# Kernel tuning notes

Measured on AMD Instinct MI355X. Metric: run time of the kernel, lower is better.

The kernel has to match this reference:

```python
import jax, jax.numpy as jnp
import numpy as np

B, D, C = 8192, 128, 1000
EPS = 1e-6      # torch nn.PairwiseDistance default eps (added to the difference)
LAMBD = 0.1


def setup_inputs() -> dict:
    key = jax.random.key(0)
    k1, k2, k3 = jax.random.split(key, 3)
    return {
        "data": jax.random.normal(k1, (B, C), jnp.float32),
        "x": jax.random.normal(k2, (B, D), jnp.float32),
        "y": jax.random.randint(k3, (B,), 0, C),
    }


def _pdist_matrix(x):
    # torch PairwiseDistance(p=2): ||x_i - x_j + eps||_2, computed without
    # materializing the [B,B,D] difference tensor.
    sq = jnp.sum(x * x, axis=1)          # [B]
    s = jnp.sum(x, axis=1)               # [B]
    n = x.shape[1]
    g = x @ x.T                          # [B,B] Gram
    d2 = (sq[:, None] + sq[None, :] - 2.0 * g
          + 2.0 * EPS * (s[:, None] - s[None, :]) + n * EPS * EPS)
    return jnp.sqrt(jnp.maximum(d2, 0.0))


def reference(data, x, y):
    # cross-entropy (mean reduction, as nn.CrossEntropyLoss default)
    logp = jax.nn.log_softmax(data, axis=-1)
    loss_acc = -jnp.mean(jnp.take_along_axis(logp, y[:, None], axis=1))

    dist = _pdist_matrix(x)                       # [B,B]
    same = y[:, None] == y[None, :]               # label mask
    first_pos = jnp.argmax(same, axis=1)          # first index with same label (pos[0] in torch)
    d_pos = jnp.take_along_axis(dist, first_pos[:, None], axis=1)[:, 0]  # [B]
    d_tot = jnp.sum(dist, axis=1)                 # [B]
    loss_feature = jnp.sum(d_pos / (d_tot - d_pos))

    loss = loss_acc + LAMBD * loss_feature
    return (loss, loss_acc, loss_feature)
```

## Files before the change

### kernel.cpp

```cpp
#include <hip/hip_runtime.h>
#include <math.h>

#define B 8192
#define D 128
#define C 1000
#define EPS 1e-6f
#define LAMBD 0.1f

#define OFF_DTOT 2
#define OFF_E (2 + B)
#define OFF_F (2 + 2 * B)
#define OFF_DPOS (2 + 3 * B)
#define OFF_FO (2 + 4 * B)
#define OFF_XBF 33792

typedef __attribute__((ext_vector_type(8))) short short8;
typedef __attribute__((ext_vector_type(4))) float floatx4;

__device__ inline unsigned short f2bf(float f) {
    union { float f; unsigned u; } v; v.f = f;
    unsigned u = v.u;
    return (unsigned short)((u + 0x7fffu + ((u >> 16) & 1u)) >> 16);
}

__global__ void __launch_bounds__(256)
k_rowstats(const float* __restrict__ x, const int* __restrict__ y, float* ws) {
    int row = blockIdx.x * 4 + (threadIdx.x >> 6);
    int lane = threadIdx.x & 63;
    const float2* x2 = (const float2*)x;
    float2 v = x2[row * 64 + lane];
    float sq = v.x * v.x + v.y * v.y;
    float s = v.x + v.y;
    for (int o = 32; o; o >>= 1) {
        sq += __shfl_xor(sq, o);
        s += __shfl_xor(s, o);
    }
    ushort2 p = { f2bf(v.x), f2bf(v.y) };
    ushort2* xrow = (ushort2*)((unsigned short*)(ws + OFF_XBF) + row * 128);
    xrow[(((lane >> 2) ^ (row & 7)) << 2) + (lane & 3)] = p;
    if (lane == 0) {
        ws[OFF_E + row] = sq + 2.f * EPS * s;
        ws[OFF_F + row] = sq - 2.f * EPS * s;
        atomicMin((unsigned*)(ws + OFF_FO) + y[row], (unsigned)row);
    }
}

__global__ void __launch_bounds__(256)
k_ce(const float* __restrict__ data, const int* __restrict__ y, float* ws) {
    int row = blockIdx.x * 4 + (threadIdx.x >> 6);
    int lane = threadIdx.x & 63;
    const float* dr = data + (size_t)row * C;
    const float4* dr4 = (const float4*)dr;

    float4 v[4];
    float m = -1e30f;
#pragma unroll
    for (int k = 0; k < 4; k++) {
        int idx = k * 64 + lane;
        if (idx < C / 4) {
            v[k] = dr4[idx];
            m = fmaxf(fmaxf(fmaxf(m, v[k].x), fmaxf(v[k].y, v[k].z)), v[k].w);
        }
    }
    for (int o = 32; o; o >>= 1) m = fmaxf(m, __shfl_xor(m, o));

    float sum = 0.f;
#pragma unroll
    for (int k = 0; k < 4; k++) {
        int idx = k * 64 + lane;
        if (idx < C / 4) {
            sum += __expf(v[k].x - m) + __expf(v[k].y - m) +
                   __expf(v[k].z - m) + __expf(v[k].w - m);
        }
    }
    for (int o = 32; o; o >>= 1) sum += __shfl_xor(sum, o);

    __shared__ float sp[4];
    if (lane == 0) {
        float lse = m + __logf(sum);
        sp[threadIdx.x >> 6] = lse - dr[y[row]];
    }
    __syncthreads();
    if (threadIdx.x == 0)
        atomicAdd(ws + 0, sp[0] + sp[1] + sp[2] + sp[3]);
}

__global__ void k_dpos(const float* __restrict__ x, const int* __restrict__ y,
                       float* ws) {
    int row = blockIdx.x * 4 + (threadIdx.x >> 6);
    int lane = threadIdx.x & 63;
    const unsigned* fo = (const unsigned*)(ws + OFF_FO);
    int fp = (int)fo[y[row]];
    float d0 = x[row * D + lane] - x[fp * D + lane] + EPS;
    float d1 = x[row * D + 64 + lane] - x[fp * D + 64 + lane] + EPS;
    float sq = d0 * d0 + d1 * d1;
    for (int o = 32; o; o >>= 1) sq += __shfl_xor(sq, o);
    if (lane == 0) ws[OFF_DPOS + row] = sqrtf(sq);
}

__global__ void __launch_bounds__(256, 2)
k_gram_dtot(float* ws) {
    const int t = threadIdx.x;
    const int lane = t & 63, wid = t >> 6;
    const int wm = wid >> 1, wn = wid & 1;
    const int lo = lane & 15, hi = lane >> 4;
    const int p = blockIdx.x >> 4;
    const int sub = blockIdx.x & 15;
    const int b0 = p, b1 = 63 - p;
    const int n0 = 64 - b0;

    const short8* __restrict__ xb8 = (const short8*)(ws + OFF_XBF);
    const float* __restrict__ e = ws + OFF_E;
    const float* __restrict__ f = ws + OFF_F;
    float* dtot = ws + OFF_DTOT;
    const float deps2 = (float)D * EPS * EPS;
    const int swz = lo & 7;

    short8 af[4][4];
    float er[4][4], rs[4][4];
    int cur_band = -1;

#define FLUSH_RS()                                                            \
    {                                                                         \
        _Pragma("unroll") for (int mr = 0; mr < 4; ++mr)                      \
            _Pragma("unroll") for (int rg = 0; rg < 4; ++rg) {                \
            float v = rs[mr][rg];                                             \
            v += __shfl_xor(v, 1);                                            \
            v += __shfl_xor(v, 2);                                            \
            v += __shfl_xor(v, 4);                                            \
            v += __shfl_xor(v, 8);                                            \
            if (lo == 0)                                                      \
                atomicAdd(&dtot[cur_band * 128 + wm * 64 + mr * 16 + hi * 4 + rg], v); \
        }                                                                     \
    }

    for (int q = sub; q < 65; q += 16) {
        int band = (q < n0) ? b0 : b1;
        int j = (q < n0) ? b0 + q : b1 + (q - n0);

        if (band != cur_band) {
            if (cur_band >= 0) FLUSH_RS();
            cur_band = band;
#pragma unroll
            for (int mr = 0; mr < 4; ++mr) {
                int r = band * 128 + wm * 64 + mr * 16 + lo;
#pragma unroll
                for (int kt = 0; kt < 4; ++kt)
                    af[kt][mr] = xb8[r * 16 + ((kt * 4 + hi) ^ swz)];
#pragma unroll
                for (int rg = 0; rg < 4; ++rg) {
                    er[mr][rg] =
                        e[band * 128 + wm * 64 + mr * 16 + hi * 4 + rg] + deps2;
                    rs[mr][rg] = 0.f;
                }
            }
        }

        const int jr = j * 128 + wn * 64;
        float fc[4];
#pragma unroll
        for (int nr = 0; nr < 4; ++nr) fc[nr] = f[jr + nr * 16 + lo];

        floatx4 acc[4][4];
#pragma unroll
        for (int mr = 0; mr < 4; ++mr)
#pragma unroll
            for (int nr = 0; nr < 4; ++nr)
                acc[mr][nr] = (floatx4){0.f, 0.f, 0.f, 0.f};

#pragma unroll
        for (int kt = 0; kt < 4; ++kt) {
            short8 bg[4];
#pragma unroll
            for (int nr = 0; nr < 4; ++nr) {
                int r = jr + nr * 16 + lo;
                bg[nr] = xb8[r * 16 + ((kt * 4 + hi) ^ swz)];
            }
#pragma unroll
            for (int mr = 0; mr < 4; ++mr)
#pragma unroll
                for (int nr = 0; nr < 4; ++nr)
                    acc[mr][nr] = __builtin_amdgcn_mfma_f32_16x16x32_bf16(
                        af[kt][mr], bg[nr], acc[mr][nr], 0, 0, 0);
        }

        float cs[4] = {0.f, 0.f, 0.f, 0.f};
#pragma unroll
        for (int mr = 0; mr < 4; ++mr)
#pragma unroll
            for (int nr = 0; nr < 4; ++nr)
#pragma unroll
                for (int rg = 0; rg < 4; ++rg) {
                    float d2 = fmaf(-2.f, acc[mr][nr][rg], er[mr][rg]) + fc[nr];
                    float pp = fmaxf(d2, deps2);
                    float d = pp * __frsqrt_rn(pp);
                    rs[mr][rg] += d;
                    cs[nr] += d;
                }

        if (j != band) {
#pragma unroll
            for (int nr = 0; nr < 4; ++nr) {
                float v = cs[nr];
                v += __shfl_xor(v, 16);
                v += __shfl_xor(v, 32);
                if (hi == 0) atomicAdd(&dtot[jr + nr * 16 + lo], v);
            }
        }
    }
    if (cur_band >= 0) FLUSH_RS();
#undef FLUSH_RS
}

__global__ void __launch_bounds__(1024)
k_featout(const float* __restrict__ ws, float* __restrict__ out) {
    int t = threadIdx.x;
    const float* dtot = ws + OFF_DTOT;
    const float* dpos = ws + OFF_DPOS;
    float r = 0.f;
#pragma unroll
    for (int k = 0; k < B / 1024; k++) {
        int i = k * 1024 + t;
        float dp = dpos[i], dt = dtot[i];
        r += dp / (dt - dp);
    }
    for (int o = 32; o; o >>= 1) r += __shfl_xor(r, o);
    __shared__ float sm[16];
    if ((t & 63) == 0) sm[t >> 6] = r;
    __syncthreads();
    if (t == 0) {
        float lf = 0.f;
#pragma unroll
        for (int w = 0; w < 16; w++) lf += sm[w];
        float la = ws[0] / (float)B;
        out[0] = la + LAMBD * lf;
        out[1] = la;
        out[2] = lf;
    }
}

extern "C" void kernel_launch(void* const* d_in, const int* in_sizes, int n_in,
                              void* d_out, int out_size, void* d_ws, size_t ws_size,
                              hipStream_t stream) {
    const float* data = (const float*)d_in[0];
    const float* x = (const float*)d_in[1];
    const int* y = (const int*)d_in[2];
    float* out = (float*)d_out;
    float* ws = (float*)d_ws;

    (void)hipMemsetAsync(ws, 0, (2 + B) * sizeof(float), stream);
    (void)hipMemsetAsync(ws + OFF_FO, 0xFF, C * sizeof(unsigned), stream);
    k_rowstats<<<B / 4, 256, 0, stream>>>(x, y, ws);
    k_ce<<<B / 4, 256, 0, stream>>>(data, y, ws);
    k_dpos<<<B / 4, 256, 0, stream>>>(x, y, ws);
    k_gram_dtot<<<512, 256, 0, stream>>>(ws);
    k_featout<<<1, 1024, 0, stream>>>(ws, out);
}
```

Measured before the change: 152.5 us.

## Drop A-fragment register caching, raise gram occupancy and grid, fold memset into rowstats

The Gram/distance kernel now reloads the A fragments on every tile and flushes the row sums per tile, no longer keeping them resident across a band. This frees registers, which allows three blocks per CU and a 768-block grid with a 24-way split over tile pairs. The bf16 XOR swizzle on stores and loads is removed, and the separate memset of the accumulators is replaced by zeroing inside k_rowstats. The cost is extra global loads and more atomics per tile, plus possible bank or channel conflicts without the swizzle.

```diff
diff --git a/kernel.cpp b/kernel.cpp
--- a/kernel.cpp
+++ b/kernel.cpp
@@ -37,12 +37,14 @@
     }
     ushort2 p = { f2bf(v.x), f2bf(v.y) };
     ushort2* xrow = (ushort2*)((unsigned short*)(ws + OFF_XBF) + row * 128);
-    xrow[(((lane >> 2) ^ (row & 7)) << 2) + (lane & 3)] = p;
+    xrow[lane] = p;
     if (lane == 0) {
         ws[OFF_E + row] = sq + 2.f * EPS * s;
         ws[OFF_F + row] = sq - 2.f * EPS * s;
         atomicMin((unsigned*)(ws + OFF_FO) + y[row], (unsigned)row);
     }
+    if (lane == 1) ws[OFF_DTOT + row] = 0.f;
+    if (blockIdx.x == 0 && threadIdx.x == 0) ws[0] = 0.f;
 }
 
 __global__ void __launch_bounds__(256)
@@ -98,14 +100,14 @@
     if (lane == 0) ws[OFF_DPOS + row] = sqrtf(sq);
 }
 
-__global__ void __launch_bounds__(256, 2)
+__global__ void __launch_bounds__(256, 3)
 k_gram_dtot(float* ws) {
     const int t = threadIdx.x;
     const int lane = t & 63, wid = t >> 6;
     const int wm = wid >> 1, wn = wid & 1;
     const int lo = lane & 15, hi = lane >> 4;
-    const int p = blockIdx.x >> 4;
-    const int sub = blockIdx.x & 15;
+    const int p = blockIdx.x / 24;
+    const int sub = blockIdx.x % 24;
     const int b0 = p, b1 = 63 - p;
     const int n0 = 64 - b0;
 
@@ -114,52 +116,12 @@
     const float* __restrict__ f = ws + OFF_F;
     float* dtot = ws + OFF_DTOT;
     const float deps2 = (float)D * EPS * EPS;
-    const int swz = lo & 7;
-
-    short8 af[4][4];
-    float er[4][4], rs[4][4];
-    int cur_band = -1;
-
-#define FLUSH_RS()                                                            \
-    {                                                                         \
-        _Pragma("unroll") for (int mr = 0; mr < 4; ++mr)                      \
-            _Pragma("unroll") for (int rg = 0; rg < 4; ++rg) {                \
-            float v = rs[mr][rg];                                             \
-            v += __shfl_xor(v, 1);                                            \
-            v += __shfl_xor(v, 2);                                            \
-            v += __shfl_xor(v, 4);                                            \
-            v += __shfl_xor(v, 8);                                            \
-            if (lo == 0)                                                      \
-                atomicAdd(&dtot[cur_band * 128 + wm * 64 + mr * 16 + hi * 4 + rg], v); \
-        }                                                                     \
-    }
-
-    for (int q = sub; q < 65; q += 16) {
-        int band = (q < n0) ? b0 : b1;
-        int j = (q < n0) ? b0 + q : b1 + (q - n0);
-
-        if (band != cur_band) {
-            if (cur_band >= 0) FLUSH_RS();
-            cur_band = band;
-#pragma unroll
-            for (int mr = 0; mr < 4; ++mr) {
-                int r = band * 128 + wm * 64 + mr * 16 + lo;
-#pragma unroll
-                for (int kt = 0; kt < 4; ++kt)
-                    af[kt][mr] = xb8[r * 16 + ((kt * 4 + hi) ^ swz)];
-#pragma unroll
-                for (int rg = 0; rg < 4; ++rg) {
-                    er[mr][rg] =
-                        e[band * 128 + wm * 64 + mr * 16 + hi * 4 + rg] + deps2;
-                    rs[mr][rg] = 0.f;
-                }
-            }
-        }
-
+
+    for (int q = sub; q < 65; q += 24) {
+        const int band = (q < n0) ? b0 : b1;
+        const int j = (q < n0) ? b0 + q : b1 + (q - n0);
+        const int ar = band * 128 + wm * 64;
         const int jr = j * 128 + wn * 64;
-        float fc[4];
-#pragma unroll
-        for (int nr = 0; nr < 4; ++nr) fc[nr] = f[jr + nr * 16 + lo];
 
         floatx4 acc[4][4];
 #pragma unroll
@@ -170,21 +132,38 @@
 
 #pragma unroll
         for (int kt = 0; kt < 4; ++kt) {
-            short8 bg[4];
-#pragma unroll
-            for (int nr = 0; nr < 4; ++nr) {
-                int r = jr + nr * 16 + lo;
-                bg[nr] = xb8[r * 16 + ((kt * 4 + hi) ^ swz)];
-            }
+            const int ch = kt * 4 + hi;
+            short8 af[4], bg[4];
+#pragma unroll
+            for (int mr = 0; mr < 4; ++mr)
+                af[mr] = xb8[(ar + mr * 16 + lo) * 16 + ch];
+#pragma unroll
+            for (int nr = 0; nr < 4; ++nr)
+                bg[nr] = xb8[(jr + nr * 16 + lo) * 16 + ch];
 #pragma unroll
             for (int mr = 0; mr < 4; ++mr)
 #pragma unroll
                 for (int nr = 0; nr < 4; ++nr)
                     acc[mr][nr] = __builtin_amdgcn_mfma_f32_16x16x32_bf16(
-                        af[kt][mr], bg[nr], acc[mr][nr], 0, 0, 0);
-        }
-
+                        af[mr], bg[nr], acc[mr][nr], 0, 0, 0);
+        }
+
+        float er[4][4], fc[4];
+#pragma unroll
+        for (int mr = 0; mr < 4; ++mr)
+#pragma unroll
+            for (int rg = 0; rg < 4; ++rg)
+                er[mr][rg] = e[ar + mr * 16 + hi * 4 + rg] + deps2;
+#pragma unroll
+        for (int nr = 0; nr < 4; ++nr) fc[nr] = f[jr + nr * 16 + lo];
+
+        float rs[4][4];
         float cs[4] = {0.f, 0.f, 0.f, 0.f};
+#pragma unroll
+        for (int mr = 0; mr < 4; ++mr)
+#pragma unroll
+            for (int rg = 0; rg < 4; ++rg) rs[mr][rg] = 0.f;
+
 #pragma unroll
         for (int mr = 0; mr < 4; ++mr)
 #pragma unroll
@@ -198,6 +177,17 @@
                     cs[nr] += d;
                 }
 
+#pragma unroll
+        for (int mr = 0; mr < 4; ++mr)
+#pragma unroll
+            for (int rg = 0; rg < 4; ++rg) {
+                float v = rs[mr][rg];
+                v += __shfl_xor(v, 1);
+                v += __shfl_xor(v, 2);
+                v += __shfl_xor(v, 4);
+                v += __shfl_xor(v, 8);
+                if (lo == 0) atomicAdd(&dtot[ar + mr * 16 + hi * 4 + rg], v);
+            }
         if (j != band) {
 #pragma unroll
             for (int nr = 0; nr < 4; ++nr) {
@@ -208,8 +198,6 @@
             }
         }
     }
-    if (cur_band >= 0) FLUSH_RS();
-#undef FLUSH_RS
 }
 
 __global__ void __launch_bounds__(1024)
@@ -248,11 +236,10 @@
     float* out = (float*)d_out;
     float* ws = (float*)d_ws;
 
-    (void)hipMemsetAsync(ws, 0, (2 + B) * sizeof(float), stream);
     (void)hipMemsetAsync(ws + OFF_FO, 0xFF, C * sizeof(unsigned), stream);
     k_rowstats<<<B / 4, 256, 0, stream>>>(x, y, ws);
     k_ce<<<B / 4, 256, 0, stream>>>(data, y, ws);
     k_dpos<<<B / 4, 256, 0, stream>>>(x, y, ws);
-    k_gram_dtot<<<512, 256, 0, stream>>>(ws);
+    k_gram_dtot<<<768, 256, 0, stream>>>(ws);
     k_featout<<<1, 1024, 0, stream>>>(ws, out);
 }
```

Result: slower. 170.1 us (+11.5%).

## Software-pipeline B-fragment loads in gram kernel and fold memset into rowstats

Applied to the files above, without the earlier changes.

Restructures the Gram/dtot loop so each K-slice of the B fragments is loaded one step ahead of its MFMA group, double-buffered in registers, and prefetches the next tile's first slice when the band is unchanged. The XOR swizzle on the bf16 copy of x is removed. The dtot/loss zeroing memset is folded into the rowstats kernel, and the workspace offsets are moved so e is 16-byte aligned and can be read as a float4. The occupancy hint in launch_bounds is dropped, which lets the compiler use more registers for the prefetch buffers but may lower waves per SIMD.

```diff
diff --git a/kernel.cpp b/kernel.cpp
--- a/kernel.cpp
+++ b/kernel.cpp
@@ -7,11 +7,11 @@
 #define EPS 1e-6f
 #define LAMBD 0.1f
 
-#define OFF_DTOT 2
-#define OFF_E (2 + B)
-#define OFF_F (2 + 2 * B)
-#define OFF_DPOS (2 + 3 * B)
-#define OFF_FO (2 + 4 * B)
+#define OFF_DTOT 16
+#define OFF_E (16 + B)
+#define OFF_F (16 + 2 * B)
+#define OFF_DPOS (16 + 3 * B)
+#define OFF_FO (16 + 4 * B)
 #define OFF_XBF 33792
 
 typedef __attribute__((ext_vector_type(8))) short short8;
@@ -37,12 +37,14 @@
     }
     ushort2 p = { f2bf(v.x), f2bf(v.y) };
     ushort2* xrow = (ushort2*)((unsigned short*)(ws + OFF_XBF) + row * 128);
-    xrow[(((lane >> 2) ^ (row & 7)) << 2) + (lane & 3)] = p;
+    xrow[lane] = p;
     if (lane == 0) {
         ws[OFF_E + row] = sq + 2.f * EPS * s;
         ws[OFF_F + row] = sq - 2.f * EPS * s;
         atomicMin((unsigned*)(ws + OFF_FO) + y[row], (unsigned)row);
     }
+    if (lane == 1) ws[OFF_DTOT + row] = 0.f;
+    if (blockIdx.x == 0 && threadIdx.x == 0) ws[0] = 0.f;
 }
 
 __global__ void __launch_bounds__(256)
@@ -98,7 +100,7 @@
     if (lane == 0) ws[OFF_DPOS + row] = sqrtf(sq);
 }
 
-__global__ void __launch_bounds__(256, 2)
+__global__ void __launch_bounds__(256)
 k_gram_dtot(float* ws) {
     const int t = threadIdx.x;
     const int lane = t & 63, wid = t >> 6;
@@ -114,11 +116,10 @@
     const float* __restrict__ f = ws + OFF_F;
     float* dtot = ws + OFF_DTOT;
     const float deps2 = (float)D * EPS * EPS;
-    const int swz = lo & 7;
 
     short8 af[4][4];
-    float er[4][4], rs[4][4];
-    int cur_band = -1;
+    short8 bgs[2][4];
+    float rs[4][4];
 
 #define FLUSH_RS()                                                            \
     {                                                                         \
@@ -129,76 +130,93 @@
             v += __shfl_xor(v, 2);                                            \
             v += __shfl_xor(v, 4);                                            \
             v += __shfl_xor(v, 8);                                            \
-            if (lo == 0)                                                      \
-                atomicAdd(&dtot[cur_band * 128 + wm * 64 + mr * 16 + hi * 4 + rg], v); \
+            if (lo == 0) atomicAdd(&dtot[ar + mr * 16 + hi * 4 + rg], v);     \
         }                                                                     \
     }
-
-    for (int q = sub; q < 65; q += 16) {
-        int band = (q < n0) ? b0 : b1;
-        int j = (q < n0) ? b0 + q : b1 + (q - n0);
-
-        if (band != cur_band) {
-            if (cur_band >= 0) FLUSH_RS();
-            cur_band = band;
-#pragma unroll
-            for (int mr = 0; mr < 4; ++mr) {
-                int r = band * 128 + wm * 64 + mr * 16 + lo;
-#pragma unroll
-                for (int kt = 0; kt < 4; ++kt)
-                    af[kt][mr] = xb8[r * 16 + ((kt * 4 + hi) ^ swz)];
+#define LOAD_AF_RS()                                                          \
+    {                                                                         \
+        _Pragma("unroll") for (int mr = 0; mr < 4; ++mr) {                    \
+            int r16 = (ar + mr * 16 + lo) * 16;                               \
+            _Pragma("unroll") for (int kt = 0; kt < 4; ++kt)                  \
+                af[kt][mr] = xb8[r16 + kt * 4 + hi];                          \
+            _Pragma("unroll") for (int rg = 0; rg < 4; ++rg) rs[mr][rg] = 0.f;\
+        }                                                                     \
+    }
+#define MFMA_GROUP(KT, BG)                                                    \
+    _Pragma("unroll") for (int mr = 0; mr < 4; ++mr)                          \
+        _Pragma("unroll") for (int nr = 0; nr < 4; ++nr)                      \
+            acc[mr][nr] = __builtin_amdgcn_mfma_f32_16x16x32_bf16(            \
+                af[KT][mr], (BG)[nr], acc[mr][nr], 0, 0, 0);
+
+    int q = sub;
+    int cur_band = (q < n0) ? b0 : b1;
+    int j = (q < n0) ? b0 + q : b1 + (q - n0);
+    int ar = cur_band * 128 + wm * 64;
+    int jr = j * 128 + wn * 64;
+
+    LOAD_AF_RS();
+#pragma unroll
+    for (int nr = 0; nr < 4; ++nr)
+        bgs[0][nr] = xb8[(jr + nr * 16 + lo) * 16 + hi];
+
+    while (true) {
+        float fc[4];
+#pragma unroll
+        for (int nr = 0; nr < 4; ++nr) fc[nr] = f[jr + nr * 16 + lo];
+        floatx4 er4[4];
+#pragma unroll
+        for (int mr = 0; mr < 4; ++mr)
+            er4[mr] = *(const floatx4*)&e[ar + mr * 16 + hi * 4];
+
+        int nq = q + 16;
+        bool have_next = (nq < 65);
+        int nband = 0, nj = 0, njr = 0;
+        if (have_next) {
+            nband = (nq < n0) ? b0 : b1;
+            nj = (nq < n0) ? b0 + nq : b1 + (nq - n0);
+            njr = nj * 128 + wn * 64;
+        }
+
+        floatx4 acc[4][4];
+#pragma unroll
+        for (int mr = 0; mr < 4; ++mr)
+#pragma unroll
+            for (int nr = 0; nr < 4; ++nr)
+                acc[mr][nr] = (floatx4){0.f, 0.f, 0.f, 0.f};
+
+#pragma unroll
+        for (int nr = 0; nr < 4; ++nr)
+            bgs[1][nr] = xb8[(jr + nr * 16 + lo) * 16 + 4 + hi];
+        MFMA_GROUP(0, bgs[0]);
+#pragma unroll
+        for (int nr = 0; nr < 4; ++nr)
+            bgs[0][nr] = xb8[(jr + nr * 16 + lo) * 16 + 8 + hi];
+        MFMA_GROUP(1, bgs[1]);
+#pragma unroll
+        for (int nr = 0; nr < 4; ++nr)
+            bgs[1][nr] = xb8[(jr + nr * 16 + lo) * 16 + 12 + hi];
+        MFMA_GROUP(2, bgs[0]);
+        if (have_next && nband == cur_band) {
+#pragma unroll
+            for (int nr = 0; nr < 4; ++nr)
+                bgs[0][nr] = xb8[(njr + nr * 16 + lo) * 16 + hi];
+        }
+        MFMA_GROUP(3, bgs[1]);
+
+        float cs[4] = {0.f, 0.f, 0.f, 0.f};
+#pragma unroll
+        for (int mr = 0; mr < 4; ++mr)
+#pragma unroll
+            for (int nr = 0; nr < 4; ++nr)
 #pragma unroll
                 for (int rg = 0; rg < 4; ++rg) {
-                    er[mr][rg] =
-                        e[band * 128 + wm * 64 + mr * 16 + hi * 4 + rg] + deps2;
-                    rs[mr][rg] = 0.f;
-                }
-            }
-        }
-
-        const int jr = j * 128 + wn * 64;
-        float fc[4];
-#pragma unroll
-        for (int nr = 0; nr < 4; ++nr) fc[nr] = f[jr + nr * 16 + lo];
-
-        floatx4 acc[4][4];
-#pragma unroll
-        for (int mr = 0; mr < 4; ++mr)
-#pragma unroll
-            for (int nr = 0; nr < 4; ++nr)
-                acc[mr][nr] = (floatx4){0.f, 0.f, 0.f, 0.f};
-
-#pragma unroll
-        for (int kt = 0; kt < 4; ++kt) {
-            short8 bg[4];
-#pragma unroll
-            for (int nr = 0; nr < 4; ++nr) {
-                int r = jr + nr * 16 + lo;
-                bg[nr] = xb8[r * 16 + ((kt * 4 + hi) ^ swz)];
-            }
-#pragma unroll
-            for (int mr = 0; mr < 4; ++mr)
-#pragma unroll
-                for (int nr = 0; nr < 4; ++nr)
-                    acc[mr][nr] = __builtin_amdgcn_mfma_f32_16x16x32_bf16(
-                        af[kt][mr], bg[nr], acc[mr][nr], 0, 0, 0);
-        }
-
-        float cs[4] = {0.f, 0.f, 0.f, 0.f};
-#pragma unroll
-        for (int mr = 0; mr < 4; ++mr)
-#pragma unroll
-            for (int nr = 0; nr < 4; ++nr)
-#pragma unroll
-                for (int rg = 0; rg < 4; ++rg) {
-                    float d2 = fmaf(-2.f, acc[mr][nr][rg], er[mr][rg]) + fc[nr];
+                    float d2 = fmaf(-2.f, acc[mr][nr][rg], er4[mr][rg] + deps2) + fc[nr];
                     float pp = fmaxf(d2, deps2);
                     float d = pp * __frsqrt_rn(pp);
                     rs[mr][rg] += d;
                     cs[nr] += d;
                 }
-
-        if (j != band) {
+        if (j != cur_band) {
 #pragma unroll
             for (int nr = 0; nr < 4; ++nr) {
                 float v = cs[nr];
@@ -207,9 +225,23 @@
                 if (hi == 0) atomicAdd(&dtot[jr + nr * 16 + lo], v);
             }
         }
-    }
-    if (cur_band >= 0) FLUSH_RS();
+
+        if (!have_next) break;
+        q = nq; j = nj; jr = njr;
+        if (nband != cur_band) {
+            FLUSH_RS();
+            cur_band = nband;
+            ar = cur_band * 128 + wm * 64;
+            LOAD_AF_RS();
+#pragma unroll
+            for (int nr = 0; nr < 4; ++nr)
+                bgs[0][nr] = xb8[(jr + nr * 16 + lo) * 16 + hi];
+        }
+    }
+    FLUSH_RS();
 #undef FLUSH_RS
+#undef LOAD_AF_RS
+#undef MFMA_GROUP
 }
 
 __global__ void __launch_bounds__(1024)
@@ -248,7 +280,6 @@
     float* out = (float*)d_out;
     float* ws = (float*)d_ws;
 
-    (void)hipMemsetAsync(ws, 0, (2 + B) * sizeof(float), stream);
     (void)hipMemsetAsync(ws + OFF_FO, 0xFF, C * sizeof(unsigned), stream);
     k_rowstats<<<B / 4, 256, 0, stream>>>(x, y, ws);
     k_ce<<<B / 4, 256, 0, stream>>>(data, y, ws);
```

Result: slower. 161.7 us (+6.0%).
